# Performance work log

Measured on AMD Instinct MI355X. Metric: run time of the kernel, lower is better.

The kernel has to match this reference:

```python
import jax, jax.numpy as jnp
import numpy as np

N, E, C, H = 20000, 320000, 128, 8
DH = C // H
CUTOFF = 5.0
LN_EPS = 1e-5


def _xavier(k, fan_in, fan_out):
    lim = np.sqrt(6.0 / (fan_in + fan_out))
    return jax.random.uniform(k, (fan_in, fan_out), jnp.float32, -lim, lim)


def setup_inputs() -> dict:
    key = jax.random.key(0)
    ks = jax.random.split(key, 24)
    s = jax.random.normal(ks[0], (N, 1, C), jnp.float32)
    v = 0.1 * jax.random.normal(ks[1], (N, 3, C), jnp.float32)
    dir_ij = jax.random.normal(ks[2], (E, 3), jnp.float32)
    dir_ij = dir_ij / (jnp.linalg.norm(dir_ij, axis=-1, keepdims=True) + 1e-9)
    d_ij = jax.random.uniform(ks[3], (E,), jnp.float32, 0.0, CUTOFF)
    r_ij = 0.5 * jax.random.normal(ks[4], (E, C), jnp.float32)
    edge_index = jax.random.randint(ks[5], (2, E), 0, N, jnp.int64 if jax.config.jax_enable_x64 else jnp.int32)
    zb = lambda n: jnp.zeros((n,), jnp.float32)
    return {
        's': s, 'v': v, 'dir_ij': dir_ij, 'd_ij': d_ij, 'r_ij': r_ij,
        'edge_index': edge_index,
        'ln_g': jnp.ones((C,), jnp.float32), 'ln_b': zb(C),
        'Wq': _xavier(ks[6], C, C), 'bq': zb(C),
        'Wk': _xavier(ks[7], C, C), 'bk': zb(C),
        'Wg1': _xavier(ks[8], C, C), 'bg1': zb(C),
        'Wg2': _xavier(ks[9], C, 3 * C), 'bg2': zb(3 * C),
        'Wv1': _xavier(ks[10], C, C), 'bv1': zb(C),
        'Wv2': _xavier(ks[11], C, 3 * C), 'bv2': zb(3 * C),
        'Wre': _xavier(ks[12], C, C), 'bre': zb(C),
        'Wra': _xavier(ks[13], C, 3 * C), 'bra': zb(3 * C),
    }


def _layernorm(x, g, b):
    m = jnp.mean(x, axis=-1, keepdims=True)
    var = jnp.mean((x - m) ** 2, axis=-1, keepdims=True)
    return (x - m) * jax.lax.rsqrt(var + LN_EPS) * g + b


def _cosine_cutoff(d):
    return 0.5 * (jnp.cos(d * (np.pi / CUTOFF)) + 1.0) * (d < CUTOFF).astype(d.dtype)


def _segment_softmax(logits, seg, n):
    # logits: [E, H], seg: [E]
    m = jax.ops.segment_max(logits, seg, num_segments=n)
    m = jnp.where(jnp.isfinite(m), m, 0.0)
    e = jnp.exp(logits - m[seg])
    z = jax.ops.segment_sum(e, seg, num_segments=n)
    return e / (z[seg] + 1e-16)


def reference(s, v, dir_ij, d_ij, r_ij, edge_index,
              ln_g, ln_b, Wq, bq, Wk, bk, Wg1, bg1, Wg2, bg2,
              Wv1, bv1, Wv2, bv2, Wre, bre, Wra, bra):
    src, dst = edge_index[0], edge_index[1]  # PyG: x_j = x[src], x_i = x[dst]
    s_ln = _layernorm(s, ln_g, ln_b)          # [N,1,C]
    s2 = s_ln[:, 0, :]                         # [N,C]

    q = (s2 @ Wq + bq).reshape(N, H, DH)
    k = (s2 @ Wk + bk).reshape(N, H, DH)
    x3 = jax.nn.silu(s2 @ Wg1 + bg1) @ Wg2 + bg2   # gamma_s -> [N,3C]
    val = jax.nn.silu(s2 @ Wv1 + bv1) @ Wv2 + bv2  # gamma_v -> [N,3C]
    r_attn = jax.nn.silu(r_ij @ Wre + bre).reshape(E, H, DH)
    r_proj = r_ij @ Wra + bra                      # [E,3C]

    # attention logits and segment softmax over destination nodes
    alpha = jnp.einsum('ehd,ehd->eh', q[dst] * k[src], r_attn) if False else jnp.sum(q[dst] * k[src] * r_attn, axis=-1)  # [E,H]
    attn = _segment_softmax(alpha, dst, N)         # [E,H]

    sea = (attn[:, :, None] * val[src].reshape(E, H, 3 * DH)).reshape(E, 3 * C)
    saa = r_proj * x3[src] * _cosine_cutoff(d_ij)[:, None]
    msg = saa + sea                                # [E,3C]
    o_s, o_d, o_v = jnp.split(msg, 3, axis=-1)     # each [E,C]

    su = jax.ops.segment_sum(o_s, dst, num_segments=N)   # [N,C]
    v_msg = dir_ij[:, :, None] * o_d[:, None, :] + o_v[:, None, :] * v[src]  # [E,3,C]
    vu = jax.ops.segment_sum(v_msg, dst, num_segments=N)  # [N,3,C]

    s_out = s_ln + su[:, None, :]
    v_out = v + vu
    return s_out, v_out, r_ij  # last_layer=True returns f_ij unchanged
```

## Files before the change

kernel.cpp:

```cpp
#include <hip/hip_runtime.h>
#include <cstdint>
#include <cstddef>

#define N_NODES 20000
#define N_EDGES 320000

typedef __attribute__((ext_vector_type(8))) short short8;
typedef __attribute__((ext_vector_type(4))) float floatx4;

__device__ __forceinline__ unsigned short f2bf(float f){
  union { float f; unsigned int i; } v; v.f = f;
  unsigned int u = v.i;
  return (unsigned short)((u + 0x7FFFu + ((u >> 16) & 1u)) >> 16);
}
__device__ __forceinline__ float bf2f(unsigned short u){
  union { unsigned int i; float f; } v; v.i = ((unsigned int)u) << 16; return v.f;
}
__device__ __forceinline__ float siluf(float x){ return x / (1.f + __expf(-x)); }
__device__ __forceinline__ short8 ld_frag16(const unsigned short* p){
  uint4 u = *(const uint4*)p;
  return *(short8*)&u;
}
__device__ __forceinline__ int clampi(int x, int lo, int hi){ return min(max(x, lo), hi); }
__device__ __forceinline__ short8 f32_to_frag(const float* p){
  float4 a = *(const float4*)p;
  float4 b = *(const float4*)(p + 4);
  short8 f;
  f[0] = (short)f2bf(a.x); f[1] = (short)f2bf(a.y);
  f[2] = (short)f2bf(a.z); f[3] = (short)f2bf(a.w);
  f[4] = (short)f2bf(b.x); f[5] = (short)f2bf(b.y);
  f[6] = (short)f2bf(b.z); f[7] = (short)f2bf(b.w);
  return f;
}

__global__ void k_pack(const float* Wq, const float* Wk,
                       const float* Wg1, const float* Wv1,
                       const float* Wg2, const float* Wv2,
                       const float* Wre, const float* Wra,
                       const float* bq, const float* bk,
                       const float* bg1, const float* bv1,
                       const float* bg2, const float* bv2,
                       const float* bre, const float* bra,
                       unsigned short* B1p, unsigned short* Wg2p, unsigned short* Wv2p,
                       unsigned short* Wep,
                       float* bias1, float* biasg2, float* biasv2, float* biase,
                       int* hist)
{
  int tid = blockIdx.x * blockDim.x + threadIdx.x;
  if (tid < 229376){
    int idx, region;
    if (tid < 65536){ region = 0; idx = tid; }
    else if (tid < 114688){ region = 1; idx = tid - 65536; }
    else if (tid < 163840){ region = 2; idx = tid - 114688; }
    else { region = 3; idx = tid - 163840; }
    int j = idx & 7, lane = (idx >> 3) & 63, kk = (idx >> 9) & 3, c = idx >> 11;
    int k = kk*32 + (lane >> 4)*8 + j;
    int n = c*16 + (lane & 15);
    if (region == 0){
      float v = (n < 128) ? Wq[k*128 + n]
              : (n < 256) ? Wk[k*128 + n - 128]
              : (n < 384) ? Wg1[k*128 + n - 256]
              : Wv1[k*128 + n - 384];
      B1p[idx] = f2bf(v);
    } else if (region == 1){ Wg2p[idx] = f2bf(Wg2[k*384 + n]); }
    else if (region == 2){ Wv2p[idx] = f2bf(Wv2[k*384 + n]); }
    else {
      float v = (n < 128) ? Wre[k*128 + n] : Wra[k*384 + n - 128];
      Wep[idx] = f2bf(v);
    }
  }
  if (tid < 512){
    bias1[tid] = tid<128 ? bq[tid] : tid<256 ? bk[tid-128] : tid<384 ? bg1[tid-256] : bv1[tid-384];
    biase[tid] = tid<128 ? bre[tid] : bra[tid-128];
  }
  if (tid < 384){ biasg2[tid] = bg2[tid]; biasv2[tid] = bv2[tid]; }
  if (tid < N_NODES) hist[tid] = 0;
}

__global__ void k_ln(const float* s_in, const float* g, const float* b,
                     unsigned short* s2b)
{
  int wid = threadIdx.x >> 6, lane = threadIdx.x & 63;
  int n = blockIdx.x*4 + wid;
  if (n >= N_NODES) return;
  const float* row = s_in + (size_t)n*128;
  float2 xv = *(const float2*)(row + lane*2);
  float x0 = xv.x, x1 = xv.y;
  float s = x0 + x1, ss = x0*x0 + x1*x1;
  for (int m = 1; m <= 32; m <<= 1){ s += __shfl_xor(s, m); ss += __shfl_xor(ss, m); }
  float mean = s * (1.f/128.f);
  float var = ss * (1.f/128.f) - mean*mean;
  float rs = rsqrtf(var + 1e-5f);
  int ch = lane*2;
  float y0 = (x0-mean)*rs*g[ch]   + b[ch];
  float y1 = (x1-mean)*rs*g[ch+1] + b[ch+1];
  ushort2 ov; ov.x = f2bf(y0); ov.y = f2bf(y1);
  *(ushort2*)(s2b + (size_t)n*128 + ch) = ov;
}

__global__ void k_hist(const int* ei, int* hist){
  int e = blockIdx.x*blockDim.x + threadIdx.x;
  if (e < N_EDGES){
    int d = clampi(ei[N_EDGES + e], 0, N_NODES-1);
    atomicAdd(&hist[d], 1);
  }
}

__global__ void k_scan(const int* hist, int* row_start, int* cursor){
  __shared__ int wsum[17];
  __shared__ int carry_s;
  int tid = threadIdx.x, lane = tid & 63, wid = tid >> 6;
  if (tid == 0) carry_s = 0;
  __syncthreads();
  for (int base = 0; base < N_NODES; base += 1024){
    int i = base + tid;
    int v = (i < N_NODES) ? hist[i] : 0;
    int incl = v;
    for (int off = 1; off < 64; off <<= 1){
      int t = __shfl_up(incl, off);
      if (lane >= off) incl += t;
    }
    if (lane == 63) wsum[wid] = incl;
    __syncthreads();
    if (tid == 0){
      int acc = carry_s;
      for (int w2 = 0; w2 < 16; w2++){ int t = wsum[w2]; wsum[w2] = acc; acc += t; }
      wsum[16] = acc;
    }
    __syncthreads();
    int excl = wsum[wid] + incl - v;
    if (i < N_NODES){ row_start[i] = excl; cursor[i] = excl; }
    __syncthreads();
    if (tid == 0) carry_s = wsum[16];
    __syncthreads();
  }
  if (threadIdx.x == 0) row_start[N_NODES] = carry_s;
}

__global__ void k_scatter(const int* ei, int* cursor, int* perm_s, int* src_s){
  int e = blockIdx.x*blockDim.x + threadIdx.x;
  if (e < N_EDGES){
    int d = clampi(ei[N_EDGES + e], 0, N_NODES-1);
    int pos = clampi(atomicAdd(&cursor[d], 1), 0, N_EDGES-1);
    perm_s[pos] = e;
    src_s[pos] = clampi(ei[e], 0, N_NODES-1);
  }
}

__global__ void __launch_bounds__(256) k_ngemm1(const unsigned short* s2b, const unsigned short* B1p, const float* bias1,
                        unsigned short* q_b, unsigned short* k_b, unsigned short* h1_b, unsigned short* h2_b)
{
  int wid = threadIdx.x >> 6, lane = threadIdx.x & 63;
  int tile = blockIdx.x*4 + wid;
  if (tile >= N_NODES/16) return;
  int l15 = lane & 15, q = lane >> 4;
  int n0 = tile*16;
  const unsigned short* arow = s2b + (size_t)(n0 + l15)*128 + q*8;
  short8 af[4];
  for (int kk = 0; kk < 4; kk++) af[kk] = ld_frag16(arow + kk*32);
  for (int c = 0; c < 32; c++){
    floatx4 acc = {0.f,0.f,0.f,0.f};
    const unsigned short* bp = B1p + (size_t)(c*4)*512 + lane*8;
    for (int kk = 0; kk < 4; kk++){
      short8 bf = ld_frag16(bp + kk*512);
      acc = __builtin_amdgcn_mfma_f32_16x16x32_bf16(af[kk], bf, acc, 0, 0, 0);
    }
    int col = c*16 + l15;
    float bias = bias1[col];
    unsigned short* dst; int cc;
    if      (c < 8){  dst = q_b;  cc = col; }
    else if (c < 16){ dst = k_b;  cc = col - 128; }
    else if (c < 24){ dst = h1_b; cc = col - 256; }
    else            { dst = h2_b; cc = col - 384; }
    bool act = (c >= 16);
    for (int r = 0; r < 4; r++){
      float vv = acc[r] + bias;
      if (act) vv = siluf(vv);
      int node = n0 + q*4 + r;
      dst[(size_t)node*128 + cc] = f2bf(vv);
    }
  }
}

__global__ void __launch_bounds__(256) k_ngemm2(const unsigned short* h1_b, const unsigned short* h2_b,
                        const unsigned short* Wg2p, const unsigned short* Wv2p,
                        const float* biasg2, const float* biasv2,
                        unsigned short* x3_b, unsigned short* val_b)
{
  int wid = threadIdx.x >> 6, lane = threadIdx.x & 63;
  int tile = blockIdx.x*4 + wid;
  if (tile >= N_NODES/16) return;
  int l15 = lane & 15, q = lane >> 4;
  int n0 = tile*16;
  for (int ph = 0; ph < 2; ph++){
    const unsigned short* srcm = ph ? h2_b : h1_b;
    const unsigned short* Wp   = ph ? Wv2p : Wg2p;
    const float* bs            = ph ? biasv2 : biasg2;
    unsigned short* dst        = ph ? val_b : x3_b;
    const unsigned short* arow = srcm + (size_t)(n0 + l15)*128 + q*8;
    short8 af[4];
    for (int kk = 0; kk < 4; kk++) af[kk] = ld_frag16(arow + kk*32);
    for (int c = 0; c < 24; c++){
      floatx4 acc = {0.f,0.f,0.f,0.f};
      const unsigned short* bp = Wp + (size_t)(c*4)*512 + lane*8;
      for (int kk = 0; kk < 4; kk++){
        short8 bf = ld_frag16(bp + kk*512);
        acc = __builtin_amdgcn_mfma_f32_16x16x32_bf16(af[kk], bf, acc, 0, 0, 0);
      }
      int col = c*16 + l15;
      float bias = bs[col];
      for (int r = 0; r < 4; r++){
        float vv = acc[r] + bias;
        int node = n0 + q*4 + r;
        dst[(size_t)node*384 + col] = f2bf(vv);
      }
    }
  }
}

__global__ void __launch_bounds__(256) k_alpha(const float* r_ij, const unsigned short* q_b, const unsigned short* k_b,
                       const unsigned short* Wep, const float* biase,
                       const int* row_start, const int* perm_s, const int* src_s,
                       float* alpha_s, float* r_out)
{
  int wid = threadIdx.x >> 6, lane = threadIdx.x & 63;
  int n = blockIdx.x*4 + wid;
  int l15 = lane & 15, q = lane >> 4;
  int rs = clampi(row_start[n], 0, N_EDGES);
  int re = clampi(row_start[n+1], rs, N_EDGES);
  if (re <= rs) return;
  for (int c0 = rs; c0 < re; c0 += 16){
    int iA = min(c0 + l15, re-1);
    bool validA = (c0 + l15 < re);
    int pA = clampi(perm_s[iA], 0, N_EDGES-1);
    const float* ar = r_ij + (size_t)pA*128 + q*8;
    float*       wr = r_out + (size_t)pA*128 + q*8;
    short8 af[4];
    for (int kk = 0; kk < 4; kk++){
      float4 a0 = *(const float4*)(ar + kk*32);
      float4 a1 = *(const float4*)(ar + kk*32 + 4);
      if (validA){ *(float4*)(wr + kk*32) = a0; *(float4*)(wr + kk*32 + 4) = a1; }
      short8 f;
      f[0]=(short)f2bf(a0.x); f[1]=(short)f2bf(a0.y); f[2]=(short)f2bf(a0.z); f[3]=(short)f2bf(a0.w);
      f[4]=(short)f2bf(a1.x); f[5]=(short)f2bf(a1.y); f[6]=(short)f2bf(a1.z); f[7]=(short)f2bf(a1.w);
      af[kk] = f;
    }
    int sv[4]; int er_[4]; bool vr[4];
    for (int r = 0; r < 4; r++){
      int e = c0 + q*4 + r;
      vr[r] = (e < re);
      int ec = min(e, re-1);
      er_[r] = e;
      sv[r] = clampi(src_s[ec], 0, N_NODES-1);
    }
    for (int c = 0; c < 8; c++){
      floatx4 acc = {0.f,0.f,0.f,0.f};
      const unsigned short* bp = Wep + (size_t)(c*4)*512 + lane*8;
      for (int kk = 0; kk < 4; kk++){
        short8 bf = ld_frag16(bp + kk*512);
        acc = __builtin_amdgcn_mfma_f32_16x16x32_bf16(af[kk], bf, acc, 0, 0, 0);
      }
      float bias = biase[c*16 + l15];
      float qv = bf2f(q_b[(size_t)n*128 + c*16 + l15]);
      float t0[4];
      for (int r = 0; r < 4; r++){
        float kvv = bf2f(k_b[(size_t)sv[r]*128 + c*16 + l15]);
        t0[r] = siluf(acc[r] + bias) * qv * kvv;
      }
      for (int m = 1; m <= 8; m <<= 1)
        for (int r = 0; r < 4; r++) t0[r] += __shfl_xor(t0[r], m);
      if (l15 == 0){
        for (int r = 0; r < 4; r++)
          if (vr[r]) alpha_s[(size_t)er_[r]*8 + c] = t0[r];
      }
    }
  }
}

__global__ void __launch_bounds__(256) k_msg(const float* s_in, const float* v_in,
                     const float* dir_ij, const float* d_ij,
                     const float* r_ij,
                     const float* ln_g, const float* ln_b,
                     const unsigned short* x3_b, const unsigned short* val_b,
                     const unsigned short* Wep, const float* biase,
                     const int* row_start, const int* perm_s, const int* src_s,
                     const float* alpha_s,
                     float* out_s, float* out_v)
{
  int wid = threadIdx.x >> 6, lane = threadIdx.x & 63;
  int n = blockIdx.x*4 + wid;
  int l15 = lane & 15, q = lane >> 4;
  int rs = clampi(row_start[n], 0, N_EDGES);
  int re = clampi(row_start[n+1], rs, N_EDGES);

  float accS[2] = {0.f, 0.f};
  float accV[6] = {0.f,0.f,0.f,0.f,0.f,0.f};

  int lh = lane & 7, lr = lane >> 3;
  float mh = -1e30f;
  for (int i = rs + lr; i < re; i += 8) mh = fmaxf(mh, alpha_s[(size_t)i*8 + lh]);
  for (int m = 8; m <= 32; m <<= 1) mh = fmaxf(mh, __shfl_xor(mh, m));
  float zh = 0.f;
  for (int i = rs + lr; i < re; i += 8) zh += __expf(alpha_s[(size_t)i*8 + lh] - mh);
  for (int m = 8; m <= 32; m <<= 1) zh += __shfl_xor(zh, m);
  float zinv = 1.f / (zh + 1e-16f);

  for (int c0 = rs; c0 < re; c0 += 16){
    int iA = min(c0 + l15, re-1);
    int pA = clampi(perm_s[iA], 0, N_EDGES-1);
    const float* ar = r_ij + (size_t)pA*128 + q*8;
    short8 af[4];
    for (int kk = 0; kk < 4; kk++){
      float4 a0 = *(const float4*)(ar + kk*32);
      float4 a1 = *(const float4*)(ar + kk*32 + 4);
      short8 f;
      f[0]=(short)f2bf(a0.x); f[1]=(short)f2bf(a0.y); f[2]=(short)f2bf(a0.z); f[3]=(short)f2bf(a0.w);
      f[4]=(short)f2bf(a1.x); f[5]=(short)f2bf(a1.y); f[6]=(short)f2bf(a1.z); f[7]=(short)f2bf(a1.w);
      af[kk] = f;
    }

    int er_[4]; int sv[4]; float cc[4]; float dv[3][4]; bool vr[4];
    for (int r = 0; r < 4; r++){
      int e = c0 + q*4 + r;
      vr[r] = (e < re);
      int ec = min(e, re-1);
      er_[r] = ec;
      sv[r] = clampi(src_s[ec], 0, N_NODES-1);
      int pr = clampi(perm_s[ec], 0, N_EDGES-1);
      float d = d_ij[pr];
      cc[r] = (vr[r] && d < 5.0f) ? 0.5f*(__cosf(d*0.6283185307179587f) + 1.f) : 0.f;
      dv[0][r] = dir_ij[pr*3+0];
      dv[1][r] = dir_ij[pr*3+1];
      dv[2][r] = dir_ij[pr*3+2];
    }
    float at4[4] = {0.f,0.f,0.f,0.f};
    for (int c = 0; c < 24; c++){
      if (c % 3 == 0){
        int h = c / 3;
        float mhc = __shfl(mh, h);
        float zic = __shfl(zinv, h);
        for (int r = 0; r < 4; r++)
          at4[r] = vr[r] ? __expf(alpha_s[(size_t)er_[r]*8 + h] - mhc) * zic : 0.f;
      }
      floatx4 acc = {0.f,0.f,0.f,0.f};
      const unsigned short* bp = Wep + (size_t)((8+c)*4)*512 + lane*8;
      for (int kk = 0; kk < 4; kk++){
        short8 bf = ld_frag16(bp + kk*512);
        acc = __builtin_amdgcn_mfma_f32_16x16x32_bf16(af[kk], bf, acc, 0, 0, 0);
      }
      float bias = biase[128 + c*16 + l15];
      float msg[4];
      for (int r = 0; r < 4; r++){
        float xv = bf2f(x3_b[(size_t)sv[r]*384 + c*16 + l15]);
        float vv = bf2f(val_b[(size_t)sv[r]*384 + c*16 + l15]);
        msg[r] = (acc[r] + bias) * xv * cc[r] + at4[r] * vv;
      }
      if (c < 8){
        float s4 = msg[0]+msg[1]+msg[2]+msg[3];
        s4 += __shfl_xor(s4, 16); s4 += __shfl_xor(s4, 32);
        if (q == (c & 3)) accS[c >> 2] += s4;
      } else if (c < 16){
        int b = c - 8;
        for (int a = 0; a < 3; a++){
          float pa = msg[0]*dv[a][0] + msg[1]*dv[a][1] + msg[2]*dv[a][2] + msg[3]*dv[a][3];
          pa += __shfl_xor(pa, 16); pa += __shfl_xor(pa, 32);
          if (q == (b & 3)) accV[(b >> 2)*3 + a] += pa;
        }
      } else {
        int b = c - 16;
        for (int a = 0; a < 3; a++){
          float pa = 0.f;
          for (int r = 0; r < 4; r++)
            pa += msg[r] * v_in[((size_t)sv[r]*3 + a)*128 + b*16 + l15];
          pa += __shfl_xor(pa, 16); pa += __shfl_xor(pa, 32);
          if (q == (b & 3)) accV[(b >> 2)*3 + a] += pa;
        }
      }
    }
  }

  {
    int ch0 = q*16 + l15, ch1 = 64 + q*16 + l15;
    float x0 = s_in[(size_t)n*128 + ch0];
    float x1 = s_in[(size_t)n*128 + ch1];
    float sm = x0 + x1, ssq = x0*x0 + x1*x1;
    for (int m = 1; m <= 32; m <<= 1){ sm += __shfl_xor(sm, m); ssq += __shfl_xor(ssq, m); }
    float mean = sm * (1.f/128.f);
    float var = ssq * (1.f/128.f) - mean*mean;
    float rsv = rsqrtf(var + 1e-5f);
    float y0 = (x0-mean)*rsv*ln_g[ch0] + ln_b[ch0];
    float y1 = (x1-mean)*rsv*ln_g[ch1] + ln_b[ch1];
    out_s[(size_t)n*128 + ch0] = y0 + accS[0];
    out_s[(size_t)n*128 + ch1] = y1 + accS[1];
  }
  for (int t = 0; t < 6; t++){
    int b = (t/3)*4 + q;
    int a = t - (t/3)*3;
    int ch = b*16 + l15;
    size_t idx = ((size_t)n*3 + a)*128 + ch;
    out_v[idx] = v_in[idx] + accV[t];
  }
}

extern "C" void kernel_launch(void* const* d_in, const int* in_sizes, int n_in,
                              void* d_out, int out_size, void* d_ws, size_t ws_size,
                              hipStream_t stream)
{
  const float* s_in   = (const float*)d_in[0];
  const float* v_in   = (const float*)d_in[1];
  const float* dir_ij = (const float*)d_in[2];
  const float* d_ij   = (const float*)d_in[3];
  const float* r_ij   = (const float*)d_in[4];
  const int*   ei     = (const int*)d_in[5];
  const float* ln_g   = (const float*)d_in[6];
  const float* ln_b   = (const float*)d_in[7];
  const float* Wq  = (const float*)d_in[8];
  const float* bq  = (const float*)d_in[9];
  const float* Wk  = (const float*)d_in[10];
  const float* bk  = (const float*)d_in[11];
  const float* Wg1 = (const float*)d_in[12];
  const float* bg1 = (const float*)d_in[13];
  const float* Wg2 = (const float*)d_in[14];
  const float* bg2 = (const float*)d_in[15];
  const float* Wv1 = (const float*)d_in[16];
  const float* bv1 = (const float*)d_in[17];
  const float* Wv2 = (const float*)d_in[18];
  const float* bv2 = (const float*)d_in[19];
  const float* Wre = (const float*)d_in[20];
  const float* bre = (const float*)d_in[21];
  const float* Wra = (const float*)d_in[22];
  const float* bra = (const float*)d_in[23];

  float* out_s = (float*)d_out;
  float* out_v = out_s + (size_t)N_NODES*128;
  float* out_r = out_v + (size_t)N_NODES*384;

  char* w = (char*)d_ws;
  size_t off = 0;
  auto alloc = [&](size_t bytes) -> void* {
    void* p = w + off;
    off = (off + bytes + 255) & ~(size_t)255;
    return p;
  };
  char* reg0 = (char*)alloc((size_t)N_EDGES*8*4);
  unsigned short* h1_b  = (unsigned short*)reg0;
  unsigned short* h2_b  = (unsigned short*)(reg0 + (size_t)N_NODES*128*2);
  float* alpha_s        = (float*)reg0;
  unsigned short* x3_b  = (unsigned short*)alloc((size_t)N_NODES*384*2);
  unsigned short* s2b   = x3_b;
  unsigned short* val_b = (unsigned short*)alloc((size_t)N_NODES*384*2);
  unsigned short* q_b   = (unsigned short*)alloc((size_t)N_NODES*128*2);
  unsigned short* k_b   = (unsigned short*)alloc((size_t)N_NODES*128*2);
  unsigned short* B1p   = (unsigned short*)alloc(65536*2);
  unsigned short* Wg2p  = (unsigned short*)alloc(49152*2);
  unsigned short* Wv2p  = (unsigned short*)alloc(49152*2);
  unsigned short* Wep   = (unsigned short*)alloc(65536*2);
  float* bias1  = (float*)alloc(512*4);
  float* biasg2 = (float*)alloc(384*4);
  float* biasv2 = (float*)alloc(384*4);
  float* biase  = (float*)alloc(512*4);
  int* hist      = (int*)alloc((size_t)N_NODES*4);
  int* row_start = (int*)alloc((size_t)(N_NODES+1)*4);
  int* cursor    = (int*)alloc((size_t)N_NODES*4);
  int* perm_s    = (int*)alloc((size_t)N_EDGES*4);
  int* src_s     = (int*)alloc((size_t)N_EDGES*4);

  k_pack<<<896, 256, 0, stream>>>(Wq, Wk, Wg1, Wv1, Wg2, Wv2, Wre, Wra,
                                  bq, bk, bg1, bv1, bg2, bv2, bre, bra,
                                  B1p, Wg2p, Wv2p, Wep,
                                  bias1, biasg2, biasv2, biase, hist);
  k_ln<<<5000, 256, 0, stream>>>(s_in, ln_g, ln_b, s2b);
  k_hist<<<1250, 256, 0, stream>>>(ei, hist);
  k_scan<<<1, 1024, 0, stream>>>(hist, row_start, cursor);
  k_scatter<<<1250, 256, 0, stream>>>(ei, cursor, perm_s, src_s);
  k_ngemm1<<<313, 256, 0, stream>>>(s2b, B1p, bias1, q_b, k_b, h1_b, h2_b);
  k_ngemm2<<<313, 256, 0, stream>>>(h1_b, h2_b, Wg2p, Wv2p, biasg2, biasv2, x3_b, val_b);
  k_alpha<<<5000, 256, 0, stream>>>(r_ij, q_b, k_b, Wep, biase, row_start, perm_s, src_s,
                                    alpha_s, out_r);
  k_msg<<<5000, 256, 0, stream>>>(s_in, v_in, dir_ij, d_ij, r_ij, ln_g, ln_b,
                                  x3_b, val_b, Wep, biase,
                                  row_start, perm_s, src_s, alpha_s, out_s, out_v);
}
```

Baseline: 1.102 ms.

## Interleave gathered node features, pre-sort edge geometry, and compute softmax stats online

Interleaves x3 and val into one bf16 buffer so each edge gather reads both at once. Transposes v into a bf16 per-channel xyz layout built in the layernorm kernel, and writes dir/d into dst-sorted order during the scatter. Computes the segment-softmax max and normalizer online in k_alpha, so k_msg no longer makes two extra passes over alpha. The goal is fewer scattered gathers and passes in the message kernel, at the cost of extra workspace, bf16 rounding of v, and more exp work in k_alpha.

```diff
diff --git a/kernel.cpp b/kernel.cpp
--- a/kernel.cpp
+++ b/kernel.cpp
@@ -22,16 +22,6 @@
   return *(short8*)&u;
 }
 __device__ __forceinline__ int clampi(int x, int lo, int hi){ return min(max(x, lo), hi); }
-__device__ __forceinline__ short8 f32_to_frag(const float* p){
-  float4 a = *(const float4*)p;
-  float4 b = *(const float4*)(p + 4);
-  short8 f;
-  f[0] = (short)f2bf(a.x); f[1] = (short)f2bf(a.y);
-  f[2] = (short)f2bf(a.z); f[3] = (short)f2bf(a.w);
-  f[4] = (short)f2bf(b.x); f[5] = (short)f2bf(b.y);
-  f[6] = (short)f2bf(b.z); f[7] = (short)f2bf(b.w);
-  return f;
-}
 
 __global__ void k_pack(const float* Wq, const float* Wk,
                        const float* Wg1, const float* Wv1,
@@ -77,8 +67,8 @@
   if (tid < N_NODES) hist[tid] = 0;
 }
 
-__global__ void k_ln(const float* s_in, const float* g, const float* b,
-                     unsigned short* s2b)
+__global__ void k_ln(const float* s_in, const float* v_in, const float* g, const float* b,
+                     unsigned short* s2b, unsigned short* vt)
 {
   int wid = threadIdx.x >> 6, lane = threadIdx.x & 63;
   int n = blockIdx.x*4 + wid;
@@ -96,6 +86,16 @@
   float y1 = (x1-mean)*rs*g[ch+1] + b[ch+1];
   ushort2 ov; ov.x = f2bf(y0); ov.y = f2bf(y1);
   *(ushort2*)(s2b + (size_t)n*128 + ch) = ov;
+
+  float2 va = *(const float2*)(v_in + ((size_t)n*3 + 0)*128 + ch);
+  float2 vb = *(const float2*)(v_in + ((size_t)n*3 + 1)*128 + ch);
+  float2 vc = *(const float2*)(v_in + ((size_t)n*3 + 2)*128 + ch);
+  uint4 wv;
+  wv.x = (unsigned int)f2bf(va.x) | ((unsigned int)f2bf(vb.x) << 16);
+  wv.y = (unsigned int)f2bf(vc.x);
+  wv.z = (unsigned int)f2bf(va.y) | ((unsigned int)f2bf(vb.y) << 16);
+  wv.w = (unsigned int)f2bf(vc.y);
+  *(uint4*)(vt + (size_t)n*512 + (size_t)ch*4) = wv;
 }
 
 __global__ void k_hist(const int* ei, int* hist){
@@ -137,13 +137,20 @@
   if (threadIdx.x == 0) row_start[N_NODES] = carry_s;
 }
 
-__global__ void k_scatter(const int* ei, int* cursor, int* perm_s, int* src_s){
+__global__ void k_scatter(const int* ei, const float* dir_ij, const float* d_ij,
+                          int* cursor, int* perm_s, int* src_s, float* dird_s){
   int e = blockIdx.x*blockDim.x + threadIdx.x;
   if (e < N_EDGES){
     int d = clampi(ei[N_EDGES + e], 0, N_NODES-1);
     int pos = clampi(atomicAdd(&cursor[d], 1), 0, N_EDGES-1);
     perm_s[pos] = e;
     src_s[pos] = clampi(ei[e], 0, N_NODES-1);
+    float4 dd;
+    dd.x = dir_ij[(size_t)e*3 + 0];
+    dd.y = dir_ij[(size_t)e*3 + 1];
+    dd.z = dir_ij[(size_t)e*3 + 2];
+    dd.w = d_ij[e];
+    *(float4*)(dird_s + (size_t)pos*4) = dd;
   }
 }
 
@@ -185,7 +192,7 @@
 __global__ void __launch_bounds__(256) k_ngemm2(const unsigned short* h1_b, const unsigned short* h2_b,
                         const unsigned short* Wg2p, const unsigned short* Wv2p,
                         const float* biasg2, const float* biasv2,
-                        unsigned short* x3_b, unsigned short* val_b)
+                        unsigned short* xv_b)
 {
   int wid = threadIdx.x >> 6, lane = threadIdx.x & 63;
   int tile = blockIdx.x*4 + wid;
@@ -196,7 +203,6 @@
     const unsigned short* srcm = ph ? h2_b : h1_b;
     const unsigned short* Wp   = ph ? Wv2p : Wg2p;
     const float* bs            = ph ? biasv2 : biasg2;
-    unsigned short* dst        = ph ? val_b : x3_b;
     const unsigned short* arow = srcm + (size_t)(n0 + l15)*128 + q*8;
     short8 af[4];
     for (int kk = 0; kk < 4; kk++) af[kk] = ld_frag16(arow + kk*32);
@@ -212,7 +218,7 @@
       for (int r = 0; r < 4; r++){
         float vv = acc[r] + bias;
         int node = n0 + q*4 + r;
-        dst[(size_t)node*384 + col] = f2bf(vv);
+        xv_b[(((size_t)node*384 + col) << 1) + ph] = f2bf(vv);
       }
     }
   }
@@ -221,7 +227,7 @@
 __global__ void __launch_bounds__(256) k_alpha(const float* r_ij, const unsigned short* q_b, const unsigned short* k_b,
                        const unsigned short* Wep, const float* biase,
                        const int* row_start, const int* perm_s, const int* src_s,
-                       float* alpha_s, float* r_out)
+                       float* alpha_s, float* stats_s, float* r_out)
 {
   int wid = threadIdx.x >> 6, lane = threadIdx.x & 63;
   int n = blockIdx.x*4 + wid;
@@ -229,6 +235,11 @@
   int rs = clampi(row_start[n], 0, N_EDGES);
   int re = clampi(row_start[n+1], rs, N_EDGES);
   if (re <= rs) return;
+
+  float m_run[8], z_run[8];
+  #pragma unroll
+  for (int h = 0; h < 8; h++){ m_run[h] = -1e30f; z_run[h] = 0.f; }
+
   for (int c0 = rs; c0 < re; c0 += 16){
     int iA = min(c0 + l15, re-1);
     bool validA = (c0 + l15 < re);
@@ -253,9 +264,11 @@
       er_[r] = e;
       sv[r] = clampi(src_s[ec], 0, N_NODES-1);
     }
+    #pragma unroll
     for (int c = 0; c < 8; c++){
       floatx4 acc = {0.f,0.f,0.f,0.f};
       const unsigned short* bp = Wep + (size_t)(c*4)*512 + lane*8;
+      #pragma unroll
       for (int kk = 0; kk < 4; kk++){
         short8 bf = ld_frag16(bp + kk*512);
         acc = __builtin_amdgcn_mfma_f32_16x16x32_bf16(af[kk], bf, acc, 0, 0, 0);
@@ -263,28 +276,57 @@
       float bias = biase[c*16 + l15];
       float qv = bf2f(q_b[(size_t)n*128 + c*16 + l15]);
       float t0[4];
+      #pragma unroll
       for (int r = 0; r < 4; r++){
         float kvv = bf2f(k_b[(size_t)sv[r]*128 + c*16 + l15]);
         t0[r] = siluf(acc[r] + bias) * qv * kvv;
       }
       for (int m = 1; m <= 8; m <<= 1)
+        #pragma unroll
         for (int r = 0; r < 4; r++) t0[r] += __shfl_xor(t0[r], m);
       if (l15 == 0){
+        #pragma unroll
         for (int r = 0; r < 4; r++)
           if (vr[r]) alpha_s[(size_t)er_[r]*8 + c] = t0[r];
       }
+      #pragma unroll
+      for (int r = 0; r < 4; r++){
+        if (vr[r]){
+          float t = t0[r];
+          float mn = fmaxf(m_run[c], t);
+          z_run[c] = z_run[c]*__expf(m_run[c]-mn) + __expf(t-mn);
+          m_run[c] = mn;
+        }
+      }
+    }
+  }
+  #pragma unroll
+  for (int h = 0; h < 8; h++){
+    float mo = m_run[h], zo = z_run[h];
+    for (int m = 16; m <= 32; m <<= 1){
+      float m2 = __shfl_xor(mo, m), z2 = __shfl_xor(zo, m);
+      float mn = fmaxf(mo, m2);
+      zo = zo*__expf(mo-mn) + z2*__expf(m2-mn);
+      mo = mn;
+    }
+    m_run[h] = mo; z_run[h] = zo;
+  }
+  if (lane == 0){
+    #pragma unroll
+    for (int h = 0; h < 8; h++){
+      stats_s[(size_t)n*16 + h]     = m_run[h];
+      stats_s[(size_t)n*16 + 8 + h] = 1.f / (z_run[h] + 1e-16f);
     }
   }
 }
 
 __global__ void __launch_bounds__(256) k_msg(const float* s_in, const float* v_in,
-                     const float* dir_ij, const float* d_ij,
                      const float* r_ij,
                      const float* ln_g, const float* ln_b,
-                     const unsigned short* x3_b, const unsigned short* val_b,
+                     const unsigned short* xv_b, const unsigned short* vt_b,
                      const unsigned short* Wep, const float* biase,
                      const int* row_start, const int* perm_s, const int* src_s,
-                     const float* alpha_s,
+                     const float* dird_s, const float* alpha_s, const float* stats_s,
                      float* out_s, float* out_v)
 {
   int wid = threadIdx.x >> 6, lane = threadIdx.x & 63;
@@ -296,20 +338,19 @@
   float accS[2] = {0.f, 0.f};
   float accV[6] = {0.f,0.f,0.f,0.f,0.f,0.f};
 
-  int lh = lane & 7, lr = lane >> 3;
-  float mh = -1e30f;
-  for (int i = rs + lr; i < re; i += 8) mh = fmaxf(mh, alpha_s[(size_t)i*8 + lh]);
-  for (int m = 8; m <= 32; m <<= 1) mh = fmaxf(mh, __shfl_xor(mh, m));
-  float zh = 0.f;
-  for (int i = rs + lr; i < re; i += 8) zh += __expf(alpha_s[(size_t)i*8 + lh] - mh);
-  for (int m = 8; m <= 32; m <<= 1) zh += __shfl_xor(zh, m);
-  float zinv = 1.f / (zh + 1e-16f);
+  float4 st0 = *(const float4*)(stats_s + (size_t)n*16);
+  float4 st1 = *(const float4*)(stats_s + (size_t)n*16 + 4);
+  float4 st2 = *(const float4*)(stats_s + (size_t)n*16 + 8);
+  float4 st3 = *(const float4*)(stats_s + (size_t)n*16 + 12);
+  float mh_[8] = {st0.x,st0.y,st0.z,st0.w,st1.x,st1.y,st1.z,st1.w};
+  float zi_[8] = {st2.x,st2.y,st2.z,st2.w,st3.x,st3.y,st3.z,st3.w};
 
   for (int c0 = rs; c0 < re; c0 += 16){
     int iA = min(c0 + l15, re-1);
     int pA = clampi(perm_s[iA], 0, N_EDGES-1);
     const float* ar = r_ij + (size_t)pA*128 + q*8;
     short8 af[4];
+    #pragma unroll
     for (int kk = 0; kk < 4; kk++){
       float4 a0 = *(const float4*)(ar + kk*32);
       float4 a1 = *(const float4*)(ar + kk*32 + 4);
@@ -319,41 +360,48 @@
       af[kk] = f;
     }
 
-    int er_[4]; int sv[4]; float cc[4]; float dv[3][4]; bool vr[4];
+    int sv[4]; float cc[4], dv0[4], dv1[4], dv2[4];
+    float ath[4][8];
+    #pragma unroll
     for (int r = 0; r < 4; r++){
       int e = c0 + q*4 + r;
-      vr[r] = (e < re);
+      bool vrr = (e < re);
       int ec = min(e, re-1);
-      er_[r] = ec;
       sv[r] = clampi(src_s[ec], 0, N_NODES-1);
-      int pr = clampi(perm_s[ec], 0, N_EDGES-1);
-      float d = d_ij[pr];
-      cc[r] = (vr[r] && d < 5.0f) ? 0.5f*(__cosf(d*0.6283185307179587f) + 1.f) : 0.f;
-      dv[0][r] = dir_ij[pr*3+0];
-      dv[1][r] = dir_ij[pr*3+1];
-      dv[2][r] = dir_ij[pr*3+2];
-    }
-    float at4[4] = {0.f,0.f,0.f,0.f};
+      float4 dd = *(const float4*)(dird_s + (size_t)ec*4);
+      cc[r] = (vrr && dd.w < 5.0f) ? 0.5f*(__cosf(dd.w*0.6283185307179587f) + 1.f) : 0.f;
+      dv0[r] = dd.x; dv1[r] = dd.y; dv2[r] = dd.z;
+      float4 A0 = *(const float4*)(alpha_s + (size_t)ec*8);
+      float4 A1 = *(const float4*)(alpha_s + (size_t)ec*8 + 4);
+      float sc = vrr ? 1.f : 0.f;
+      ath[r][0] = __expf(A0.x - mh_[0]) * zi_[0] * sc;
+      ath[r][1] = __expf(A0.y - mh_[1]) * zi_[1] * sc;
+      ath[r][2] = __expf(A0.z - mh_[2]) * zi_[2] * sc;
+      ath[r][3] = __expf(A0.w - mh_[3]) * zi_[3] * sc;
+      ath[r][4] = __expf(A1.x - mh_[4]) * zi_[4] * sc;
+      ath[r][5] = __expf(A1.y - mh_[5]) * zi_[5] * sc;
+      ath[r][6] = __expf(A1.z - mh_[6]) * zi_[6] * sc;
+      ath[r][7] = __expf(A1.w - mh_[7]) * zi_[7] * sc;
+    }
+
+    #pragma unroll
     for (int c = 0; c < 24; c++){
-      if (c % 3 == 0){
-        int h = c / 3;
-        float mhc = __shfl(mh, h);
-        float zic = __shfl(zinv, h);
-        for (int r = 0; r < 4; r++)
-          at4[r] = vr[r] ? __expf(alpha_s[(size_t)er_[r]*8 + h] - mhc) * zic : 0.f;
-      }
+      const int h = c / 3;
       floatx4 acc = {0.f,0.f,0.f,0.f};
       const unsigned short* bp = Wep + (size_t)((8+c)*4)*512 + lane*8;
+      #pragma unroll
       for (int kk = 0; kk < 4; kk++){
         short8 bf = ld_frag16(bp + kk*512);
         acc = __builtin_amdgcn_mfma_f32_16x16x32_bf16(af[kk], bf, acc, 0, 0, 0);
       }
       float bias = biase[128 + c*16 + l15];
       float msg[4];
+      #pragma unroll
       for (int r = 0; r < 4; r++){
-        float xv = bf2f(x3_b[(size_t)sv[r]*384 + c*16 + l15]);
-        float vv = bf2f(val_b[(size_t)sv[r]*384 + c*16 + l15]);
-        msg[r] = (acc[r] + bias) * xv * cc[r] + at4[r] * vv;
+        unsigned int xv = *(const unsigned int*)(xv_b + (((size_t)sv[r]*384 + c*16 + l15) << 1));
+        float xvf = bf2f((unsigned short)(xv & 0xffffu));
+        float vvf = bf2f((unsigned short)(xv >> 16));
+        msg[r] = (acc[r] + bias) * xvf * cc[r] + ath[r][h] * vvf;
       }
       if (c < 8){
         float s4 = msg[0]+msg[1]+msg[2]+msg[3];
@@ -361,19 +409,34 @@
         if (q == (c & 3)) accS[c >> 2] += s4;
       } else if (c < 16){
         int b = c - 8;
-        for (int a = 0; a < 3; a++){
-          float pa = msg[0]*dv[a][0] + msg[1]*dv[a][1] + msg[2]*dv[a][2] + msg[3]*dv[a][3];
-          pa += __shfl_xor(pa, 16); pa += __shfl_xor(pa, 32);
-          if (q == (b & 3)) accV[(b >> 2)*3 + a] += pa;
+        float p0 = msg[0]*dv0[0] + msg[1]*dv0[1] + msg[2]*dv0[2] + msg[3]*dv0[3];
+        float p1 = msg[0]*dv1[0] + msg[1]*dv1[1] + msg[2]*dv1[2] + msg[3]*dv1[3];
+        float p2 = msg[0]*dv2[0] + msg[1]*dv2[1] + msg[2]*dv2[2] + msg[3]*dv2[3];
+        p0 += __shfl_xor(p0, 16); p0 += __shfl_xor(p0, 32);
+        p1 += __shfl_xor(p1, 16); p1 += __shfl_xor(p1, 32);
+        p2 += __shfl_xor(p2, 16); p2 += __shfl_xor(p2, 32);
+        if (q == (b & 3)){
+          accV[(b >> 2)*3 + 0] += p0;
+          accV[(b >> 2)*3 + 1] += p1;
+          accV[(b >> 2)*3 + 2] += p2;
         }
       } else {
         int b = c - 16;
-        for (int a = 0; a < 3; a++){
-          float pa = 0.f;
-          for (int r = 0; r < 4; r++)
-            pa += msg[r] * v_in[((size_t)sv[r]*3 + a)*128 + b*16 + l15];
-          pa += __shfl_xor(pa, 16); pa += __shfl_xor(pa, 32);
-          if (q == (b & 3)) accV[(b >> 2)*3 + a] += pa;
+        float p0 = 0.f, p1 = 0.f, p2 = 0.f;
+        #pragma unroll
+        for (int r = 0; r < 4; r++){
+          uint2 vv = *(const uint2*)(vt_b + (((size_t)sv[r]*128 + b*16 + l15) << 2));
+          p0 += msg[r] * bf2f((unsigned short)(vv.x & 0xffffu));
+          p1 += msg[r] * bf2f((unsigned short)(vv.x >> 16));
+          p2 += msg[r] * bf2f((unsigned short)(vv.y & 0xffffu));
+        }
+        p0 += __shfl_xor(p0, 16); p0 += __shfl_xor(p0, 32);
+        p1 += __shfl_xor(p1, 16); p1 += __shfl_xor(p1, 32);
+        p2 += __shfl_xor(p2, 16); p2 += __shfl_xor(p2, 32);
+        if (q == (b & 3)){
+          accV[(b >> 2)*3 + 0] += p0;
+          accV[(b >> 2)*3 + 1] += p1;
+          accV[(b >> 2)*3 + 2] += p2;
         }
       }
     }
@@ -446,11 +509,13 @@
   unsigned short* h1_b  = (unsigned short*)reg0;
   unsigned short* h2_b  = (unsigned short*)(reg0 + (size_t)N_NODES*128*2);
   float* alpha_s        = (float*)reg0;
-  unsigned short* x3_b  = (unsigned short*)alloc((size_t)N_NODES*384*2);
-  unsigned short* s2b   = x3_b;
-  unsigned short* val_b = (unsigned short*)alloc((size_t)N_NODES*384*2);
+  unsigned short* xv_b  = (unsigned short*)alloc((size_t)N_NODES*384*2*2);
+  unsigned short* s2b   = xv_b;
   unsigned short* q_b   = (unsigned short*)alloc((size_t)N_NODES*128*2);
   unsigned short* k_b   = (unsigned short*)alloc((size_t)N_NODES*128*2);
+  unsigned short* vt_b  = (unsigned short*)alloc((size_t)N_NODES*128*4*2);
+  float* dird_s  = (float*)alloc((size_t)N_EDGES*4*4);
+  float* stats_s = (float*)alloc((size_t)N_NODES*16*4);
   unsigned short* B1p   = (unsigned short*)alloc(65536*2);
   unsigned short* Wg2p  = (unsigned short*)alloc(49152*2);
   unsigned short* Wv2p  = (unsigned short*)alloc(49152*2);
@@ -469,15 +534,16 @@
                                   bq, bk, bg1, bv1, bg2, bv2, bre, bra,
                                   B1p, Wg2p, Wv2p, Wep,
                                   bias1, biasg2, biasv2, biase, hist);
-  k_ln<<<5000, 256, 0, stream>>>(s_in, ln_g, ln_b, s2b);
+  k_ln<<<5000, 256, 0, stream>>>(s_in, v_in, ln_g, ln_b, s2b, vt_b);
   k_hist<<<1250, 256, 0, stream>>>(ei, hist);
   k_scan<<<1, 1024, 0, stream>>>(hist, row_start, cursor);
-  k_scatter<<<1250, 256, 0, stream>>>(ei, cursor, perm_s, src_s);
+  k_scatter<<<1250, 256, 0, stream>>>(ei, dir_ij, d_ij, cursor, perm_s, src_s, dird_s);
   k_ngemm1<<<313, 256, 0, stream>>>(s2b, B1p, bias1, q_b, k_b, h1_b, h2_b);
-  k_ngemm2<<<313, 256, 0, stream>>>(h1_b, h2_b, Wg2p, Wv2p, biasg2, biasv2, x3_b, val_b);
+  k_ngemm2<<<313, 256, 0, stream>>>(h1_b, h2_b, Wg2p, Wv2p, biasg2, biasv2, xv_b);
   k_alpha<<<5000, 256, 0, stream>>>(r_ij, q_b, k_b, Wep, biase, row_start, perm_s, src_s,
-                                    alpha_s, out_r);
-  k_msg<<<5000, 256, 0, stream>>>(s_in, v_in, dir_ij, d_ij, r_ij, ln_g, ln_b,
-                                  x3_b, val_b, Wep, biase,
-                                  row_start, perm_s, src_s, alpha_s, out_s, out_v);
-}
+                                    alpha_s, stats_s, out_r);
+  k_msg<<<5000, 256, 0, stream>>>(s_in, v_in, r_ij, ln_g, ln_b,
+                                  xv_b, vt_b, Wep, biase,
+                                  row_start, perm_s, src_s, dird_s, alpha_s, stats_s,
+                                  out_s, out_v);
+}
```

Result: slower. 2.391 ms (+117.1%).
